# Kernel optimization log

Hardware: AMD Instinct MI355X
Metric: run time of the kernel (lower is better)

## Reference

```python
import jax, jax.numpy as jnp
import numpy as np


def setup_inputs() -> dict:
    key = jax.random.key(0)
    k1, k2, k3 = jax.random.split(key, 3)
    m, n, d = 4096, 8192, 128
    sub_graph = jax.random.uniform(k1, (m, n), dtype=jnp.float32)
    sub_x = jax.random.normal(k2, (m, d), dtype=jnp.float32)
    all_x = jax.random.normal(k3, (n, d), dtype=jnp.float32)
    return {"sub_graph": sub_graph, "sub_x": sub_x, "all_x": all_x}


def reference(sub_graph, sub_x, all_x):
    # graph_loss, 2D branch. Algebraically identical to the torch code:
    #   trace(X^T diag(d) X) = sum_i d_i * ||x_i||^2
    #   trace(A^T G B)       = sum(A * (G @ B))
    # This avoids materializing the [m,m]/[n,n] diag matrices.
    row_deg = sub_graph.sum(axis=1)            # [m]
    col_deg = sub_graph.sum(axis=0)            # [n]
    term0 = jnp.sum(row_deg * jnp.sum(sub_x * sub_x, axis=1))
    term1 = jnp.sum(col_deg * jnp.sum(all_x * all_x, axis=1))
    cross = jnp.sum(sub_x * (sub_graph @ all_x))
    loss = term0 + term1 - 2.0 * cross
    m, n = sub_graph.shape
    return loss / (m * n)
```

## Files before the change

### kernel.cpp

```cpp
#include <hip/hip_runtime.h>
#include <hip/hip_bf16.h>

#define M 4096
#define N 8192
#define D 128
#define TI 128
#define TJ 128
#define LDB 136

typedef __attribute__((ext_vector_type(8))) short short8_t;
typedef __attribute__((ext_vector_type(4))) float f32x4;

__device__ inline short f2bf(float f) {
    union { float f; unsigned u; } v; v.f = f;
    unsigned r = v.u + 0x7FFFu + ((v.u >> 16) & 1u);
    return (short)(r >> 16);
}

__global__ __launch_bounds__(256) void norms_kernel(const float* __restrict__ sub_x,
                                                    const float* __restrict__ all_x,
                                                    float* __restrict__ ws,
                                                    float* __restrict__ out) {
    int wave = threadIdx.x >> 6;
    int lane = threadIdx.x & 63;
    int row  = blockIdx.x * 4 + wave;

    const float* src;
    float* dst;
    if (row < M) { src = sub_x + (size_t)row * D; dst = ws + row; }
    else         { int r = row - M; src = all_x + (size_t)r * D; dst = ws + M + r; }

    float2 v = ((const float2*)src)[lane];
    float s = v.x * v.x + v.y * v.y;
    #pragma unroll
    for (int off = 32; off > 0; off >>= 1) s += __shfl_down(s, off, 64);
    if (lane == 0) dst[0] = s;

    if (blockIdx.x == 0 && threadIdx.x == 0) out[0] = 0.0f;
}

__global__ __launch_bounds__(256, 3) void graph_loss_kernel(const float* __restrict__ G,
                                                            const float* __restrict__ sub_x,
                                                            const float* __restrict__ all_x,
                                                            const float* __restrict__ ws,
                                                            float* __restrict__ out) {
    __shared__ short Bs[TJ * LDB];
    __shared__ float red[4];

    const int tid  = threadIdx.x;
    const int lane = tid & 63;
    const int wave = tid >> 6;
    const int quad = lane >> 4;
    const int l16  = lane & 15;

    const int ti = blockIdx.x >> 6;
    const int tj = blockIdx.x & 63;
    const int i0 = ti * TI;
    const int j0 = tj * TJ;

    {
        const int tcol  = (tid & 31) * 4;
        const int trow0 = tid >> 5;
        #pragma unroll
        for (int r = 0; r < 16; ++r) {
            const int row = r * 8 + trow0;
            const float4 v = *(const float4*)(all_x + (size_t)(j0 + row) * D + tcol);
            short4 b;
            b.x = f2bf(v.x); b.y = f2bf(v.y); b.z = f2bf(v.z); b.w = f2bf(v.w);
            *(short4*)(&Bs[row * LDB + tcol]) = b;
        }
    }

    short8_t a_frag[2][4];
    #pragma unroll
    for (int s = 0; s < 2; ++s) {
        const int m = i0 + (wave * 2 + s) * 16 + l16;
        const float* ap = sub_x + (size_t)m * D + quad * 8;
        #pragma unroll
        for (int t = 0; t < 4; ++t) {
            float4 v0 = *(const float4*)(ap + t * 32);
            float4 v1 = *(const float4*)(ap + t * 32 + 4);
            short8_t f;
            f[0] = f2bf(v0.x); f[1] = f2bf(v0.y); f[2] = f2bf(v0.z); f[3] = f2bf(v0.w);
            f[4] = f2bf(v1.x); f[5] = f2bf(v1.y); f[6] = f2bf(v1.z); f[7] = f2bf(v1.w);
            a_frag[s][t] = f;
        }
    }

    __syncthreads();

    f32x4 acc[2][8];
    #pragma unroll
    for (int s = 0; s < 2; ++s)
        #pragma unroll
        for (int j = 0; j < 8; ++j)
            acc[s][j] = (f32x4){0.f, 0.f, 0.f, 0.f};

    #pragma unroll
    for (int t = 0; t < 4; ++t) {
        short8_t b_frag[8];
        #pragma unroll
        for (int j = 0; j < 8; ++j)
            b_frag[j] = *(const short8_t*)(&Bs[(j * 16 + l16) * LDB + t * 32 + quad * 8]);
        #pragma unroll
        for (int s = 0; s < 2; ++s)
            #pragma unroll
            for (int j = 0; j < 8; ++j)
                acc[s][j] = __builtin_amdgcn_mfma_f32_16x16x32_bf16(a_frag[s][t], b_frag[j],
                                                                    acc[s][j], 0, 0, 0);
    }

    const float* sxn = ws;
    const float* axn = ws + M;

    float sx[2][4];
    #pragma unroll
    for (int s = 0; s < 2; ++s)
        #pragma unroll
        for (int r = 0; r < 4; ++r)
            sx[s][r] = sxn[i0 + (wave * 2 + s) * 16 + quad * 4 + r];
    float ax[8];
    #pragma unroll
    for (int j = 0; j < 8; ++j)
        ax[j] = axn[j0 + j * 16 + l16];

    float local = 0.0f;
    #pragma unroll
    for (int s = 0; s < 2; ++s) {
        #pragma unroll
        for (int r = 0; r < 4; ++r) {
            const int row = i0 + (wave * 2 + s) * 16 + quad * 4 + r;
            const float* gp = G + (size_t)row * N + j0 + l16;
            const float sv = sx[s][r];
            #pragma unroll
            for (int j = 0; j < 8; ++j) {
                const float g = gp[j * 16];
                local += g * (sv + ax[j] - 2.0f * acc[s][j][r]);
            }
        }
    }

    #pragma unroll
    for (int off = 32; off > 0; off >>= 1) local += __shfl_down(local, off, 64);
    if (lane == 0) red[wave] = local;
    __syncthreads();
    if (tid == 0) {
        const float bsum = red[0] + red[1] + red[2] + red[3];
        atomicAdd(out, bsum * (1.0f / 33554432.0f));
    }
}

extern "C" void kernel_launch(void* const* d_in, const int* in_sizes, int n_in,
                              void* d_out, int out_size, void* d_ws, size_t ws_size,
                              hipStream_t stream) {
    const float* G      = (const float*)d_in[0];
    const float* sub_x  = (const float*)d_in[1];
    const float* all_x  = (const float*)d_in[2];
    float* out = (float*)d_out;
    float* ws  = (float*)d_ws;

    norms_kernel<<<(M + N) / 4, 256, 0, stream>>>(sub_x, all_x, ws, out);
    graph_loss_kernel<<<(M / TI) * (N / TJ), 256, 0, stream>>>(G, sub_x, all_x, ws, out);
}
```

Measured before the change: 202.7 us.

## Precompute bf16 packed operand layouts in prep kernel and switch to 32x32 MFMA

The prep kernel now also converts sub_x and all_x to bf16 once and stores them in a k-chunked, MFMA-ready layout in the workspace. The main kernel then loads the fragments directly, with no per-block fp32-to-bf16 conversion or redundant reads. It also switches from 16x16x32 to 32x32x16 MFMA and processes G one 32-column strip at a time, which lowers accumulator register pressure. The cost is extra workspace traffic in the prep kernel and a different G access pattern, with 16 row loads per strip.

```diff
diff --git a/kernel.cpp b/kernel.cpp
--- a/kernel.cpp
+++ b/kernel.cpp
@@ -4,145 +4,119 @@
 #define M 4096
 #define N 8192
 #define D 128
-#define TI 128
-#define TJ 128
-#define LDB 136
 
 typedef __attribute__((ext_vector_type(8))) short short8_t;
-typedef __attribute__((ext_vector_type(4))) float f32x4;
+typedef __attribute__((ext_vector_type(16))) float f32x16;
 
-__device__ inline short f2bf(float f) {
+__device__ inline unsigned short f2bf(float f) {
     union { float f; unsigned u; } v; v.f = f;
     unsigned r = v.u + 0x7FFFu + ((v.u >> 16) & 1u);
-    return (short)(r >> 16);
+    return (unsigned short)(r >> 16);
 }
 
-__global__ __launch_bounds__(256) void norms_kernel(const float* __restrict__ sub_x,
-                                                    const float* __restrict__ all_x,
-                                                    float* __restrict__ ws,
-                                                    float* __restrict__ out) {
-    int wave = threadIdx.x >> 6;
-    int lane = threadIdx.x & 63;
-    int row  = blockIdx.x * 4 + wave;
 
-    const float* src;
-    float* dst;
-    if (row < M) { src = sub_x + (size_t)row * D; dst = ws + row; }
-    else         { int r = row - M; src = all_x + (size_t)r * D; dst = ws + M + r; }
+__global__ __launch_bounds__(256) void prep_kernel(const float* __restrict__ sub_x,
+                                                   const float* __restrict__ all_x,
+                                                   float* __restrict__ ws,
+                                                   float* __restrict__ out) {
+    const int wave = threadIdx.x >> 6;
+    const int lane = threadIdx.x & 63;
+    const int row  = blockIdx.x * 4 + wave;
 
-    float2 v = ((const float2*)src)[lane];
+    unsigned* sxb = (unsigned*)(ws + M + N);
+    unsigned* axb = sxb + (size_t)M * 64;
+
+    const float* src; float* ndst; unsigned* tdst; int r, R;
+    if (row < M) { r = row;     src = sub_x + (size_t)r * D; ndst = ws + r;     tdst = sxb; R = M; }
+    else         { r = row - M; src = all_x + (size_t)r * D; ndst = ws + M + r; tdst = axb; R = N; }
+
+    const float2 v = ((const float2*)src)[lane];
+
     float s = v.x * v.x + v.y * v.y;
     #pragma unroll
     for (int off = 32; off > 0; off >>= 1) s += __shfl_down(s, off, 64);
-    if (lane == 0) dst[0] = s;
+    if (lane == 0) ndst[0] = s;
+
+    const unsigned p = ((unsigned)f2bf(v.y) << 16) | (unsigned)f2bf(v.x);
+    const int k8 = lane >> 2, q = lane & 3;
+    tdst[((size_t)k8 * R + r) * 4 + q] = p;
 
     if (blockIdx.x == 0 && threadIdx.x == 0) out[0] = 0.0f;
 }
 
 __global__ __launch_bounds__(256, 3) void graph_loss_kernel(const float* __restrict__ G,
-                                                            const float* __restrict__ sub_x,
-                                                            const float* __restrict__ all_x,
                                                             const float* __restrict__ ws,
                                                             float* __restrict__ out) {
-    __shared__ short Bs[TJ * LDB];
+    __shared__ uint4 Bs[16 * 128];
     __shared__ float red[4];
 
     const int tid  = threadIdx.x;
     const int lane = tid & 63;
-    const int wave = tid >> 6;
-    const int quad = lane >> 4;
-    const int l16  = lane & 15;
+    const int w    = tid >> 6;
+    const int c    = lane & 31;
+    const int hw   = lane >> 5;
 
     const int ti = blockIdx.x >> 6;
     const int tj = blockIdx.x & 63;
-    const int i0 = ti * TI;
-    const int j0 = tj * TJ;
+    const int i0 = ti * 128;
+    const int j0 = tj * 128;
 
-    {
-        const int tcol  = (tid & 31) * 4;
-        const int trow0 = tid >> 5;
-        #pragma unroll
-        for (int r = 0; r < 16; ++r) {
-            const int row = r * 8 + trow0;
-            const float4 v = *(const float4*)(all_x + (size_t)(j0 + row) * D + tcol);
-            short4 b;
-            b.x = f2bf(v.x); b.y = f2bf(v.y); b.z = f2bf(v.z); b.w = f2bf(v.w);
-            *(short4*)(&Bs[row * LDB + tcol]) = b;
-        }
+    const float* sxn = ws;
+    const float* axn = ws + M;
+    const uint4* sxb = (const uint4*)(ws + M + N);
+    const uint4* axb = sxb + (size_t)16 * M;
+
+    #pragma unroll
+    for (int rr = 0; rr < 8; ++rr) {
+        const int id  = rr * 256 + tid;
+        const int col = id & 127, k8 = id >> 7;
+        Bs[id] = axb[(size_t)k8 * N + j0 + col];
     }
 
-    short8_t a_frag[2][4];
+    short8_t a_frag[8];
     #pragma unroll
-    for (int s = 0; s < 2; ++s) {
-        const int m = i0 + (wave * 2 + s) * 16 + l16;
-        const float* ap = sub_x + (size_t)m * D + quad * 8;
-        #pragma unroll
-        for (int t = 0; t < 4; ++t) {
-            float4 v0 = *(const float4*)(ap + t * 32);
-            float4 v1 = *(const float4*)(ap + t * 32 + 4);
-            short8_t f;
-            f[0] = f2bf(v0.x); f[1] = f2bf(v0.y); f[2] = f2bf(v0.z); f[3] = f2bf(v0.w);
-            f[4] = f2bf(v1.x); f[5] = f2bf(v1.y); f[6] = f2bf(v1.z); f[7] = f2bf(v1.w);
-            a_frag[s][t] = f;
-        }
+    for (int kk = 0; kk < 8; ++kk) {
+        const uint4 t = sxb[(size_t)(kk * 2 + hw) * M + i0 + w * 32 + c];
+        a_frag[kk] = *(const short8_t*)&t;
     }
+
+    float sxv[16];
+    #pragma unroll
+    for (int r = 0; r < 16; ++r)
+        sxv[r] = sxn[i0 + w * 32 + (r & 3) + 8 * (r >> 2) + 4 * hw];
 
     __syncthreads();
 
-    f32x4 acc[2][8];
-    #pragma unroll
-    for (int s = 0; s < 2; ++s)
-        #pragma unroll
-        for (int j = 0; j < 8; ++j)
-            acc[s][j] = (f32x4){0.f, 0.f, 0.f, 0.f};
+    float local = 0.0f;
 
     #pragma unroll
-    for (int t = 0; t < 4; ++t) {
-        short8_t b_frag[8];
+    for (int jt = 0; jt < 4; ++jt) {
+        const float* gbase = G + (size_t)(i0 + w * 32 + 4 * hw) * N + j0 + jt * 32 + c;
+        float gv[16];
         #pragma unroll
-        for (int j = 0; j < 8; ++j)
-            b_frag[j] = *(const short8_t*)(&Bs[(j * 16 + l16) * LDB + t * 32 + quad * 8]);
+        for (int r = 0; r < 16; ++r)
+            gv[r] = gbase[(size_t)((r & 3) + 8 * (r >> 2)) * N];
+
+        const float axv = axn[j0 + jt * 32 + c];
+
+        f32x16 acc;
         #pragma unroll
-        for (int s = 0; s < 2; ++s)
-            #pragma unroll
-            for (int j = 0; j < 8; ++j)
-                acc[s][j] = __builtin_amdgcn_mfma_f32_16x16x32_bf16(a_frag[s][t], b_frag[j],
-                                                                    acc[s][j], 0, 0, 0);
-    }
+        for (int r = 0; r < 16; ++r) acc[r] = 0.0f;
 
-    const float* sxn = ws;
-    const float* axn = ws + M;
+        #pragma unroll
+        for (int kk = 0; kk < 8; ++kk) {
+            const short8_t b = *(const short8_t*)&Bs[(kk * 2 + hw) * 128 + jt * 32 + c];
+            acc = __builtin_amdgcn_mfma_f32_32x32x16_bf16(a_frag[kk], b, acc, 0, 0, 0);
+        }
 
-    float sx[2][4];
-    #pragma unroll
-    for (int s = 0; s < 2; ++s)
         #pragma unroll
-        for (int r = 0; r < 4; ++r)
-            sx[s][r] = sxn[i0 + (wave * 2 + s) * 16 + quad * 4 + r];
-    float ax[8];
-    #pragma unroll
-    for (int j = 0; j < 8; ++j)
-        ax[j] = axn[j0 + j * 16 + l16];
-
-    float local = 0.0f;
-    #pragma unroll
-    for (int s = 0; s < 2; ++s) {
-        #pragma unroll
-        for (int r = 0; r < 4; ++r) {
-            const int row = i0 + (wave * 2 + s) * 16 + quad * 4 + r;
-            const float* gp = G + (size_t)row * N + j0 + l16;
-            const float sv = sx[s][r];
-            #pragma unroll
-            for (int j = 0; j < 8; ++j) {
-                const float g = gp[j * 16];
-                local += g * (sv + ax[j] - 2.0f * acc[s][j][r]);
-            }
-        }
+        for (int r = 0; r < 16; ++r)
+            local += gv[r] * (sxv[r] + axv - 2.0f * acc[r]);
     }
 
     #pragma unroll
     for (int off = 32; off > 0; off >>= 1) local += __shfl_down(local, off, 64);
-    if (lane == 0) red[wave] = local;
+    if (lane == 0) red[w] = local;
     __syncthreads();
     if (tid == 0) {
         const float bsum = red[0] + red[1] + red[2] + red[3];
@@ -159,6 +133,6 @@
     float* out = (float*)d_out;
     float* ws  = (float*)d_ws;
 
-    norms_kernel<<<(M + N) / 4, 256, 0, stream>>>(sub_x, all_x, ws, out);
-    graph_loss_kernel<<<(M / TI) * (N / TJ), 256, 0, stream>>>(G, sub_x, all_x, ws, out);
+    prep_kernel<<<(M + N) / 4, 256, 0, stream>>>(sub_x, all_x, ws, out);
+    graph_loss_kernel<<<(M / 128) * (N / 128), 256, 0, stream>>>(G, ws, out);
 }
```

Result: no change. 203.5 us (+0.4%).
